# Kernel tuning notes

Hardware: AMD Instinct MI355X
Metric: run time of the kernel (lower is better)

## Reference

```python
import jax, jax.numpy as jnp
import numpy as np

B = 32768      # batch of pooled BEATs embeddings
D = 768        # d_model
H = 64         # bottleneck
E = 7          # number of machine types (experts)


def setup_inputs() -> dict:
    key = jax.random.key(0)
    k_x, k_id, k_w1, k_b1, k_w2, k_b2 = jax.random.split(key, 6)
    x = jax.random.normal(k_x, (B, D), dtype=jnp.float32)
    expert_ids = jax.random.randint(k_id, (B,), 0, E, dtype=jnp.int64)
    # per-expert bottleneck adapter params (Linear(D,H) -> ReLU -> Linear(H,D))
    s1 = 1.0 / np.sqrt(D)
    s2 = 1.0 / np.sqrt(H)
    W1 = jax.random.uniform(k_w1, (E, D, H), jnp.float32, -s1, s1)
    b1 = jax.random.uniform(k_b1, (E, H), jnp.float32, -s1, s1)
    W2 = jax.random.uniform(k_w2, (E, H, D), jnp.float32, -s2, s2)
    b2 = jax.random.uniform(k_b2, (E, D), jnp.float32, -s2, s2)
    return {"x": x, "expert_ids": expert_ids, "W1": W1, "b1": b1, "W2": W2, "b2": b2}


def reference(x, expert_ids, W1, b1, W2, b2):
    # out[i] = x[i] + adapter_{id[i]}(x[i]); hard one-hot routing.
    # E is small and fixed, so loop over experts and mask-select (vectorized over batch).
    out = x
    for e in range(E):
        h = jax.nn.relu(x @ W1[e] + b1[e])          # [B, H]
        y = h @ W2[e] + b2[e]                        # [B, D]
        mask = (expert_ids == e)[:, None]            # [B, 1]
        out = out + jnp.where(mask, y, jnp.zeros((), x.dtype))
    return out
```

## Files before the change

### kernel.cpp

```cpp
#include <hip/hip_runtime.h>

#define B_ROWS 32768
#define D_DIM 768
#define H_DIM 64
#define E_NUM 7
#define BM 64
#define PERM_CAP (B_ROWS + E_NUM * BM)
#define NBLOCKS_MAIN (PERM_CAP / BM)
#define W_ELEMS (E_NUM * D_DIM * H_DIM)

#define PREP_INIT ((PERM_CAP + 255) / 256)
#define PREP_W1 (E_NUM * 24)
#define PREP_W2 (E_NUM * 12)

#define WS_COUNTS 0
#define WS_BASE   64
#define WS_CURSOR 128
#define WS_PERM   256
#define WS_W      133120
#define WS_WF     1376256
#define WS_NEEDED (WS_W + 2 * WS_WF)

typedef __attribute__((ext_vector_type(8))) short short8;
typedef __attribute__((ext_vector_type(8))) __bf16 bf16x8;
typedef __attribute__((ext_vector_type(4))) float f32x4;

__device__ __forceinline__ unsigned short f2bf(float f) {
  unsigned int u = __float_as_uint(f);
  unsigned int r = (u + 0x7fffu + ((u >> 16) & 1u)) >> 16;
  return (unsigned short)r;
}
__device__ __forceinline__ float bf2f(unsigned short s) {
  return __uint_as_float(((unsigned int)s) << 16);
}
__device__ __forceinline__ f32x4 mfma16(short8 a, short8 b, f32x4 c) {
  return __builtin_amdgcn_mfma_f32_16x16x32_bf16(
      __builtin_bit_cast(bf16x8, a), __builtin_bit_cast(bf16x8, b), c, 0, 0, 0);
}

__global__ void k_prep(int* __restrict__ counts, int* __restrict__ perm,
                       const float* __restrict__ W1, const float* __restrict__ W2,
                       short* __restrict__ w1f, short* __restrict__ w2f) {
  __shared__ __align__(16) float tile[64][65];
  const int bid = blockIdx.x;
  const int t = threadIdx.x;

  if (bid < PREP_INIT) {
    int i = bid * 256 + t;
    if (i < PERM_CAP) perm[i] = -1;
    if (bid == 0 && t < 16) counts[t] = 0;
    return;
  }
  if (bid < PREP_INIT + PREP_W1) {
    const int b = bid - PREP_INIT;
    const int e = b / 24, kt = b % 24;
    {
      const int d = t >> 3, hc = (t & 7) * 8;
      const float* src = W1 + ((size_t)(e * D_DIM + kt * 32 + d)) * H_DIM + hc;
      f32x4 v0 = *reinterpret_cast<const f32x4*>(src);
      f32x4 v1 = *reinterpret_cast<const f32x4*>(src + 4);
#pragma unroll
      for (int i = 0; i < 4; ++i) {
        tile[d][hc + i] = v0[i];
        tile[d][hc + 4 + i] = v1[i];
      }
    }
    __syncthreads();
    {
      const int n = t >> 6, lane = t & 63;
      const int kgo = lane >> 4, l15o = lane & 15;
      short8 hi8, lo8;
#pragma unroll
      for (int j = 0; j < 8; ++j) {
        float v = tile[kgo * 8 + j][n * 16 + l15o];
        unsigned short h = f2bf(v);
        hi8[j] = (short)h;
        lo8[j] = (short)f2bf(v - bf2f(h));
      }
      short* dst = w1f + ((size_t)(((e * 4 + n) * 24 + kt) * 2) << 9) + (lane << 3);
      *reinterpret_cast<short8*>(dst) = hi8;
      *reinterpret_cast<short8*>(dst + 512) = lo8;
    }
    return;
  }
  {
    const int b = bid - PREP_INIT - PREP_W1;
    const int e = b / 12, ctb = b % 12;
    {
      const int h = t >> 2, dc = (t & 3) * 16;
      const float* src = W2 + ((size_t)(e * H_DIM + h)) * D_DIM + ctb * 64 + dc;
#pragma unroll
      for (int k = 0; k < 4; ++k) {
        f32x4 v = *reinterpret_cast<const f32x4*>(src + k * 4);
#pragma unroll
        for (int i = 0; i < 4; ++i) tile[h][dc + k * 4 + i] = v[i];
      }
    }
    __syncthreads();
    {
      const int ct4 = t >> 6, lane = t & 63;
      const int kgo = lane >> 4, l15o = lane & 15;
      const int ct = ctb * 4 + ct4;
#pragma unroll
      for (int ks = 0; ks < 2; ++ks) {
        short8 hi8, lo8;
#pragma unroll
        for (int j = 0; j < 8; ++j) {
          float v = tile[ks * 32 + kgo * 8 + j][ct4 * 16 + l15o];
          unsigned short h = f2bf(v);
          hi8[j] = (short)h;
          lo8[j] = (short)f2bf(v - bf2f(h));
        }
        short* dst = w2f + ((size_t)(((e * 48 + ct) * 2 + ks) * 2) << 9) + (lane << 3);
        *reinterpret_cast<short8*>(dst) = hi8;
        *reinterpret_cast<short8*>(dst + 512) = lo8;
      }
    }
    return;
  }
}

__global__ void k_hist(const int* __restrict__ eid, int* __restrict__ counts) {
  __shared__ int lc[E_NUM];
  if (threadIdx.x < E_NUM) lc[threadIdx.x] = 0;
  __syncthreads();
  int e = eid[blockIdx.x * 256 + threadIdx.x];
  e = e < 0 ? 0 : (e >= E_NUM ? E_NUM - 1 : e);
  atomicAdd(&lc[e], 1);
  __syncthreads();
  if (threadIdx.x < E_NUM) atomicAdd(&counts[threadIdx.x], lc[threadIdx.x]);
}

__global__ void k_scan(const int* __restrict__ counts, int* __restrict__ base,
                       int* __restrict__ cursor) {
  if (threadIdx.x == 0) {
    int run = 0;
    for (int e = 0; e < E_NUM; ++e) {
      base[e] = run;
      cursor[e] = run;
      run += ((counts[e] + BM - 1) / BM) * BM;
    }
    base[E_NUM] = run;
  }
}

__global__ void k_scatter(const int* __restrict__ eid, int* __restrict__ cursor,
                          int* __restrict__ perm) {
  __shared__ int lc[E_NUM];
  __shared__ int lb[E_NUM];
  if (threadIdx.x < E_NUM) lc[threadIdx.x] = 0;
  __syncthreads();
  int i = blockIdx.x * 256 + threadIdx.x;
  int e = eid[i];
  e = e < 0 ? 0 : (e >= E_NUM ? E_NUM - 1 : e);
  int lpos = atomicAdd(&lc[e], 1);
  __syncthreads();
  if (threadIdx.x < E_NUM) lb[threadIdx.x] = atomicAdd(&cursor[threadIdx.x], lc[threadIdx.x]);
  __syncthreads();
  perm[lb[e] + lpos] = i;
}

__global__ __launch_bounds__(512, 4) void k_adapter(
    const float* __restrict__ x, const float* __restrict__ b1,
    const float* __restrict__ b2, const short* __restrict__ w1f,
    const short* __restrict__ w2f, const int* __restrict__ base,
    const int* __restrict__ perm, float* __restrict__ out) {
  __shared__ __align__(16) short hl_hi[4][16][72];
  __shared__ __align__(16) short hl_lo[4][16][72];
  __shared__ __align__(16) float ldsT[8][16][68];

  const int tid = threadIdx.x;
  const int wid = tid >> 6;
  const int lane = tid & 63;
  const int l15 = lane & 15;
  const int kg = lane >> 4;
  const int r = wid & 3;
  const int half = wid >> 2;
  const int m0 = blockIdx.x * BM;

  int e = 0;
#pragma unroll
  for (int i = 1; i < E_NUM; ++i)
    if (m0 >= base[i]) e = i;

  const int ar = perm[m0 + r * 16 + l15];
  const float* xrow = x + (size_t)(ar < 0 ? 0 : ar) * D_DIM;
  const short* w1e = w1f + (size_t)e * 98304;
  const int n0 = half * 2, n1 = half * 2 + 1;
#define W1P(n_, kt_) (w1e + (((size_t)((n_)*24 + (kt_)) * 2) << 9) + (lane << 3))

  f32x4 acc1[2] = {{0.f, 0.f, 0.f, 0.f}, {0.f, 0.f, 0.f, 0.f}};

  f32x4 nxa = *reinterpret_cast<const f32x4*>(xrow + kg * 8);
  f32x4 nxb = *reinterpret_cast<const f32x4*>(xrow + kg * 8 + 4);
  short8 nb0 = *reinterpret_cast<const short8*>(W1P(n0, 0));
  short8 nb1 = *reinterpret_cast<const short8*>(W1P(n0, 0) + 512);
  short8 nb2 = *reinterpret_cast<const short8*>(W1P(n1, 0));
  short8 nb3 = *reinterpret_cast<const short8*>(W1P(n1, 0) + 512);

#pragma unroll
  for (int kt = 0; kt < 24; ++kt) {
    f32x4 xa = nxa, xb = nxb;
    short8 b0h = nb0, b0l = nb1, b1h = nb2, b1l = nb3;
    if (kt < 23) {
      const int k0 = (kt + 1) * 32 + kg * 8;
      nxa = *reinterpret_cast<const f32x4*>(xrow + k0);
      nxb = *reinterpret_cast<const f32x4*>(xrow + k0 + 4);
      nb0 = *reinterpret_cast<const short8*>(W1P(n0, kt + 1));
      nb1 = *reinterpret_cast<const short8*>(W1P(n0, kt + 1) + 512);
      nb2 = *reinterpret_cast<const short8*>(W1P(n1, kt + 1));
      nb3 = *reinterpret_cast<const short8*>(W1P(n1, kt + 1) + 512);
    }
    short8 ahi, alo;
#pragma unroll
    for (int i = 0; i < 4; ++i) {
      unsigned short h0 = f2bf(xa[i]);
      ahi[i] = (short)h0;
      alo[i] = (short)f2bf(xa[i] - bf2f(h0));
      unsigned short h1 = f2bf(xb[i]);
      ahi[4 + i] = (short)h1;
      alo[4 + i] = (short)f2bf(xb[i] - bf2f(h1));
    }
    acc1[0] = mfma16(ahi, b0h, acc1[0]);
    acc1[0] = mfma16(alo, b0h, acc1[0]);
    acc1[0] = mfma16(ahi, b0l, acc1[0]);
    acc1[1] = mfma16(ahi, b1h, acc1[1]);
    acc1[1] = mfma16(alo, b1h, acc1[1]);
    acc1[1] = mfma16(ahi, b1l, acc1[1]);
  }

#pragma unroll
  for (int nn = 0; nn < 2; ++nn) {
    const int col = (half * 2 + nn) * 16 + l15;
    const float bv = b1[e * H_DIM + col];
#pragma unroll
    for (int j = 0; j < 4; ++j) {
      float v = acc1[nn][j] + bv;
      v = v > 0.f ? v : 0.f;
      unsigned short hh = f2bf(v);
      hl_hi[r][kg * 4 + j][col] = (short)hh;
      hl_lo[r][kg * 4 + j][col] = (short)f2bf(v - bf2f(hh));
    }
  }

  const short* w2e = w2f + (size_t)e * 98304;
  const int ct0 = half * 24;
#define W2P(ct_, ks_) (w2e + (((size_t)((ct_)*2 + (ks_)) * 2) << 9) + (lane << 3))
  short8 nwh = *reinterpret_cast<const short8*>(W2P(ct0, 0));
  short8 nwl = *reinterpret_cast<const short8*>(W2P(ct0, 0) + 512);

  const int grow = perm[m0 + r * 16 + (lane >> 2)];

  __syncthreads();

  short8 a2h[2], a2l[2];
#pragma unroll
  for (int ks = 0; ks < 2; ++ks) {
    a2h[ks] = *reinterpret_cast<const short8*>(&hl_hi[r][l15][ks * 32 + kg * 8]);
    a2l[ks] = *reinterpret_cast<const short8*>(&hl_lo[r][l15][ks * 32 + kg * 8]);
  }

  const float* b2e = b2 + e * D_DIM;
  const int tr = lane >> 2, cq = lane & 3;
  const float* xr2 = x + (size_t)(grow < 0 ? 0 : grow) * D_DIM;
  float* orow = out + (size_t)(grow < 0 ? 0 : grow) * D_DIM;

#pragma unroll
  for (int g = 0; g < 6; ++g) {
    f32x4 acc2[4];
#pragma unroll
    for (int t = 0; t < 8; ++t) {
      const int ct4 = t >> 1, ks = t & 1;
      short8 wh = nwh, wl = nwl;
      if (!(g == 5 && t == 7)) {
        const int t2 = t + 1;
        const int g2 = (t2 == 8) ? g + 1 : g;
        const int tt = t2 & 7;
        const int nct = ct0 + g2 * 4 + (tt >> 1);
        const int nks = tt & 1;
        nwh = *reinterpret_cast<const short8*>(W2P(nct, nks));
        nwl = *reinterpret_cast<const short8*>(W2P(nct, nks) + 512);
      }
      if (ks == 0) acc2[ct4] = (f32x4){0.f, 0.f, 0.f, 0.f};
      acc2[ct4] = mfma16(a2h[ks], wh, acc2[ct4]);
      acc2[ct4] = mfma16(a2l[ks], wh, acc2[ct4]);
      acc2[ct4] = mfma16(a2h[ks], wl, acc2[ct4]);
    }
#pragma unroll
    for (int ct4 = 0; ct4 < 4; ++ct4)
#pragma unroll
      for (int j = 0; j < 4; ++j) ldsT[wid][kg * 4 + j][ct4 * 16 + l15] = acc2[ct4][j];
    asm volatile("s_waitcnt lgkmcnt(0)" ::: "memory");
    __builtin_amdgcn_sched_barrier(0);

    const int colbase = (half * 6 + g) * 64 + cq * 16;
    f32x4 y0 = *reinterpret_cast<const f32x4*>(&ldsT[wid][tr][cq * 16 + 0]);
    f32x4 y1 = *reinterpret_cast<const f32x4*>(&ldsT[wid][tr][cq * 16 + 4]);
    f32x4 y2 = *reinterpret_cast<const f32x4*>(&ldsT[wid][tr][cq * 16 + 8]);
    f32x4 y3 = *reinterpret_cast<const f32x4*>(&ldsT[wid][tr][cq * 16 + 12]);
    if (grow >= 0) {
#pragma unroll
      for (int k = 0; k < 4; ++k) {
        f32x4 y = k == 0 ? y0 : (k == 1 ? y1 : (k == 2 ? y2 : y3));
        f32x4 bv = *reinterpret_cast<const f32x4*>(b2e + colbase + k * 4);
        f32x4 xv = *reinterpret_cast<const f32x4*>(xr2 + colbase + k * 4);
        f32x4 o = y + bv + xv;
        *reinterpret_cast<f32x4*>(orow + colbase + k * 4) = o;
      }
    }
  }
#undef W1P
#undef W2P
}

__global__ void k_fallback(const float* __restrict__ x, const int* __restrict__ eid,
                           const float* __restrict__ W1, const float* __restrict__ b1,
                           const float* __restrict__ W2, const float* __restrict__ b2,
                           float* __restrict__ out) {
  __shared__ float xs[D_DIM];
  __shared__ float hs[H_DIM];
  const int row = blockIdx.x;
  int e = eid[row];
  e = e < 0 ? 0 : (e >= E_NUM ? E_NUM - 1 : e);
  const float* xr = x + (size_t)row * D_DIM;
  for (int i = threadIdx.x; i < D_DIM; i += 256) xs[i] = xr[i];
  __syncthreads();
  if (threadIdx.x < H_DIM) {
    const float* w = W1 + (size_t)e * D_DIM * H_DIM + threadIdx.x;
    float acc = b1[e * H_DIM + threadIdx.x];
    for (int d = 0; d < D_DIM; ++d) acc += xs[d] * w[(size_t)d * H_DIM];
    hs[threadIdx.x] = acc > 0.f ? acc : 0.f;
  }
  __syncthreads();
  for (int c = threadIdx.x; c < D_DIM; c += 256) {
    const float* w = W2 + (size_t)e * H_DIM * D_DIM + c;
    float acc = b2[e * D_DIM + c];
    for (int h = 0; h < H_DIM; ++h) acc += hs[h] * w[(size_t)h * D_DIM];
    out[(size_t)row * D_DIM + c] = xs[c] + acc;
  }
}

extern "C" void kernel_launch(void* const* d_in, const int* in_sizes, int n_in,
                              void* d_out, int out_size, void* d_ws, size_t ws_size,
                              hipStream_t stream) {
  const float* x = (const float*)d_in[0];
  const int* eid = (const int*)d_in[1];
  const float* W1 = (const float*)d_in[2];
  const float* b1 = (const float*)d_in[3];
  const float* W2 = (const float*)d_in[4];
  const float* b2 = (const float*)d_in[5];
  float* out = (float*)d_out;

  if (ws_size < (size_t)WS_NEEDED) {
    k_fallback<<<B_ROWS, 256, 0, stream>>>(x, eid, W1, b1, W2, b2, out);
    return;
  }

  char* ws = (char*)d_ws;
  int* counts = (int*)(ws + WS_COUNTS);
  int* base = (int*)(ws + WS_BASE);
  int* cursor = (int*)(ws + WS_CURSOR);
  int* perm = (int*)(ws + WS_PERM);
  short* w1f = (short*)(ws + WS_W);
  short* w2f = (short*)(ws + WS_W + WS_WF);

  k_prep<<<PREP_INIT + PREP_W1 + PREP_W2, 256, 0, stream>>>(counts, perm, W1, W2, w1f, w2f);
  k_hist<<<B_ROWS / 256, 256, 0, stream>>>(eid, counts);
  k_scan<<<1, 64, 0, stream>>>(counts, base, cursor);
  k_scatter<<<B_ROWS / 256, 256, 0, stream>>>(eid, cursor, perm);
  k_adapter<<<NBLOCKS_MAIN, 512, 0, stream>>>(x, b1, b2, w1f, w2f, base, perm, out);
}
```

Before: 294.0 us.

## Use single-wave 16-row tiles with async global-to-LDS staging of x rows

Replaces the 512-thread, 64-row-tile adapter kernel with one-wavefront blocks that each process 16 gathered rows across all 64 hidden units and all 768 output columns. The gathered x rows are now staged into double-buffered, XOR-swizzled LDS using global_load_lds with explicit vmcnt waits, and W1 fragments are double-buffered in registers. The residual x values for the second GEMM are prefetched one group ahead, and the inter-wave __syncthreads is removed. Each wave now streams the full W1/W2 expert weights for just 16 rows, which raises weight traffic per row, and per-expert tile padding now costs up to 15 rows instead of 63.

```diff
diff --git a/kernel.cpp b/kernel.cpp
--- a/kernel.cpp
+++ b/kernel.cpp
@@ -4,9 +4,9 @@
 #define D_DIM 768
 #define H_DIM 64
 #define E_NUM 7
-#define BM 64
+#define BM 16
 #define PERM_CAP (B_ROWS + E_NUM * BM)
-#define NBLOCKS_MAIN (PERM_CAP / BM)
+#define NTILES (PERM_CAP / BM)
 #define W_ELEMS (E_NUM * D_DIM * H_DIM)
 
 #define PREP_INIT ((PERM_CAP + 255) / 256)
@@ -17,7 +17,7 @@
 #define WS_BASE   64
 #define WS_CURSOR 128
 #define WS_PERM   256
-#define WS_W      133120
+#define WS_W      131840
 #define WS_WF     1376256
 #define WS_NEEDED (WS_W + 2 * WS_WF)
 
@@ -36,6 +36,11 @@
 __device__ __forceinline__ f32x4 mfma16(short8 a, short8 b, f32x4 c) {
   return __builtin_amdgcn_mfma_f32_16x16x32_bf16(
       __builtin_bit_cast(bf16x8, a), __builtin_bit_cast(bf16x8, b), c, 0, 0, 0);
+}
+__device__ __forceinline__ void gload_lds16(const float* g, void* l) {
+  __builtin_amdgcn_global_load_lds(
+      (const __attribute__((address_space(1))) unsigned int*)g,
+      (__attribute__((address_space(3))) unsigned int*)l, 16, 0, 0);
 }
 
 __global__ void k_prep(int* __restrict__ counts, int* __restrict__ perm,
@@ -160,22 +165,19 @@
   perm[lb[e] + lpos] = i;
 }
 
-__global__ __launch_bounds__(512, 4) void k_adapter(
+__global__ __launch_bounds__(64, 2) void k_adapter(
     const float* __restrict__ x, const float* __restrict__ b1,
     const float* __restrict__ b2, const short* __restrict__ w1f,
     const short* __restrict__ w2f, const int* __restrict__ base,
     const int* __restrict__ perm, float* __restrict__ out) {
-  __shared__ __align__(16) short hl_hi[4][16][72];
-  __shared__ __align__(16) short hl_lo[4][16][72];
-  __shared__ __align__(16) float ldsT[8][16][68];
-
-  const int tid = threadIdx.x;
-  const int wid = tid >> 6;
-  const int lane = tid & 63;
+  __shared__ __align__(16) float stg[2][2][16][32];
+  __shared__ __align__(16) short hl_hi[16][72];
+  __shared__ __align__(16) short hl_lo[16][72];
+  __shared__ __align__(16) float ldsT[16][68];
+
+  const int lane = threadIdx.x;
   const int l15 = lane & 15;
   const int kg = lane >> 4;
-  const int r = wid & 3;
-  const int half = wid >> 2;
   const int m0 = blockIdx.x * BM;
 
   int e = 0;
@@ -183,100 +185,134 @@
   for (int i = 1; i < E_NUM; ++i)
     if (m0 >= base[i]) e = i;
 
-  const int ar = perm[m0 + r * 16 + l15];
-  const float* xrow = x + (size_t)(ar < 0 ? 0 : ar) * D_DIM;
+  const int r8 = lane >> 3;
+  int pr0 = perm[m0 + r8];
+  int pr1 = perm[m0 + 8 + r8];
+  if (pr0 < 0) pr0 = 0;
+  if (pr1 < 0) pr1 = 0;
+  const int sc = ((lane & 7) ^ r8) * 4;
+  const float* sb0 = x + (size_t)pr0 * D_DIM + sc;
+  const float* sb1 = x + (size_t)pr1 * D_DIM + sc;
+
   const short* w1e = w1f + (size_t)e * 98304;
-  const int n0 = half * 2, n1 = half * 2 + 1;
-#define W1P(n_, kt_) (w1e + (((size_t)((n_)*24 + (kt_)) * 2) << 9) + (lane << 3))
-
-  f32x4 acc1[2] = {{0.f, 0.f, 0.f, 0.f}, {0.f, 0.f, 0.f, 0.f}};
-
-  f32x4 nxa = *reinterpret_cast<const f32x4*>(xrow + kg * 8);
-  f32x4 nxb = *reinterpret_cast<const f32x4*>(xrow + kg * 8 + 4);
-  short8 nb0 = *reinterpret_cast<const short8*>(W1P(n0, 0));
-  short8 nb1 = *reinterpret_cast<const short8*>(W1P(n0, 0) + 512);
-  short8 nb2 = *reinterpret_cast<const short8*>(W1P(n1, 0));
-  short8 nb3 = *reinterpret_cast<const short8*>(W1P(n1, 0) + 512);
-
-#pragma unroll
-  for (int kt = 0; kt < 24; ++kt) {
-    f32x4 xa = nxa, xb = nxb;
-    short8 b0h = nb0, b0l = nb1, b1h = nb2, b1l = nb3;
-    if (kt < 23) {
-      const int k0 = (kt + 1) * 32 + kg * 8;
-      nxa = *reinterpret_cast<const f32x4*>(xrow + k0);
-      nxb = *reinterpret_cast<const f32x4*>(xrow + k0 + 4);
-      nb0 = *reinterpret_cast<const short8*>(W1P(n0, kt + 1));
-      nb1 = *reinterpret_cast<const short8*>(W1P(n0, kt + 1) + 512);
-      nb2 = *reinterpret_cast<const short8*>(W1P(n1, kt + 1));
-      nb3 = *reinterpret_cast<const short8*>(W1P(n1, kt + 1) + 512);
-    }
-    short8 ahi, alo;
-#pragma unroll
-    for (int i = 0; i < 4; ++i) {
-      unsigned short h0 = f2bf(xa[i]);
-      ahi[i] = (short)h0;
-      alo[i] = (short)f2bf(xa[i] - bf2f(h0));
-      unsigned short h1 = f2bf(xb[i]);
-      ahi[4 + i] = (short)h1;
-      alo[4 + i] = (short)f2bf(xb[i] - bf2f(h1));
-    }
-    acc1[0] = mfma16(ahi, b0h, acc1[0]);
-    acc1[0] = mfma16(alo, b0h, acc1[0]);
-    acc1[0] = mfma16(ahi, b0l, acc1[0]);
-    acc1[1] = mfma16(ahi, b1h, acc1[1]);
-    acc1[1] = mfma16(alo, b1h, acc1[1]);
-    acc1[1] = mfma16(ahi, b1l, acc1[1]);
-  }
-
-#pragma unroll
-  for (int nn = 0; nn < 2; ++nn) {
-    const int col = (half * 2 + nn) * 16 + l15;
+
+#define STAGE_PAIR(p)                                                      \
+  {                                                                        \
+    char* db_ = (char*)&stg[(p) & 1][0][0][0];                             \
+    const int k0_ = (p) * 64;                                              \
+    gload_lds16(sb0 + k0_, db_ + lane * 16);                               \
+    gload_lds16(sb1 + k0_, db_ + 1024 + lane * 16);                        \
+    gload_lds16(sb0 + k0_ + 32, db_ + 2048 + lane * 16);                   \
+    gload_lds16(sb1 + k0_ + 32, db_ + 3072 + lane * 16);                   \
+  }
+
+#define LOAD_W1(kt, dst)                                                   \
+  {                                                                        \
+    _Pragma("unroll") for (int n_ = 0; n_ < 4; ++n_) {                     \
+      const short* p_ =                                                    \
+          w1e + (((size_t)(n_ * 24 + (kt)) * 2) << 9) + (lane << 3);       \
+      dst[n_][0] = *reinterpret_cast<const short8*>(p_);                   \
+      dst[n_][1] = *reinterpret_cast<const short8*>(p_ + 512);             \
+    }                                                                      \
+  }
+
+#define DO_KT(kt, w_)                                                      \
+  {                                                                        \
+    const int c0_ = (kg * 2) ^ (l15 & 7);                                  \
+    const float* sp_ = &stg[((kt) >> 1) & 1][(kt)&1][l15][0];              \
+    f32x4 va_ = *reinterpret_cast<const f32x4*>(sp_ + c0_ * 4);            \
+    f32x4 vb_ = *reinterpret_cast<const f32x4*>(sp_ + (c0_ ^ 1) * 4);      \
+    short8 ahi_, alo_;                                                     \
+    _Pragma("unroll") for (int i_ = 0; i_ < 4; ++i_) {                     \
+      unsigned short h0_ = f2bf(va_[i_]);                                  \
+      ahi_[i_] = (short)h0_;                                               \
+      alo_[i_] = (short)f2bf(va_[i_] - bf2f(h0_));                         \
+      unsigned short h1_ = f2bf(vb_[i_]);                                  \
+      ahi_[4 + i_] = (short)h1_;                                           \
+      alo_[4 + i_] = (short)f2bf(vb_[i_] - bf2f(h1_));                     \
+    }                                                                      \
+    _Pragma("unroll") for (int n_ = 0; n_ < 4; ++n_) {                     \
+      acc1[n_] = mfma16(ahi_, w_[n_][0], acc1[n_]);                        \
+      acc1[n_] = mfma16(alo_, w_[n_][0], acc1[n_]);                        \
+      acc1[n_] = mfma16(ahi_, w_[n_][1], acc1[n_]);                        \
+    }                                                                      \
+  }
+
+  f32x4 acc1[4] = {{0.f, 0.f, 0.f, 0.f},
+                   {0.f, 0.f, 0.f, 0.f},
+                   {0.f, 0.f, 0.f, 0.f},
+                   {0.f, 0.f, 0.f, 0.f}};
+  short8 wA[4][2], wB[4][2];
+
+  STAGE_PAIR(0);
+  __builtin_amdgcn_sched_barrier(0);
+  LOAD_W1(0, wA);
+  __builtin_amdgcn_sched_barrier(0);
+  STAGE_PAIR(1);
+  __builtin_amdgcn_sched_barrier(0);
+
+#pragma unroll
+  for (int p = 0; p < 12; ++p) {
+    asm volatile("s_waitcnt vmcnt(12)" ::: "memory");
+    __builtin_amdgcn_sched_barrier(0);
+    LOAD_W1(2 * p + 1, wB);
+    DO_KT(2 * p, wA);
+    if (2 * p + 2 < 24) LOAD_W1(2 * p + 2, wA);
+    DO_KT(2 * p + 1, wB);
+    __builtin_amdgcn_sched_barrier(0);
+    if (p + 2 < 12) STAGE_PAIR(p + 2);
+    __builtin_amdgcn_sched_barrier(0);
+  }
+
+#pragma unroll
+  for (int nn = 0; nn < 4; ++nn) {
+    const int col = nn * 16 + l15;
     const float bv = b1[e * H_DIM + col];
 #pragma unroll
     for (int j = 0; j < 4; ++j) {
       float v = acc1[nn][j] + bv;
       v = v > 0.f ? v : 0.f;
       unsigned short hh = f2bf(v);
-      hl_hi[r][kg * 4 + j][col] = (short)hh;
-      hl_lo[r][kg * 4 + j][col] = (short)f2bf(v - bf2f(hh));
-    }
+      hl_hi[kg * 4 + j][col] = (short)hh;
+      hl_lo[kg * 4 + j][col] = (short)f2bf(v - bf2f(hh));
+    }
+  }
+
+  short8 a2h[2], a2l[2];
+#pragma unroll
+  for (int ks = 0; ks < 2; ++ks) {
+    a2h[ks] = *reinterpret_cast<const short8*>(&hl_hi[l15][ks * 32 + kg * 8]);
+    a2l[ks] = *reinterpret_cast<const short8*>(&hl_lo[l15][ks * 32 + kg * 8]);
   }
 
   const short* w2e = w2f + (size_t)e * 98304;
-  const int ct0 = half * 24;
 #define W2P(ct_, ks_) (w2e + (((size_t)((ct_)*2 + (ks_)) * 2) << 9) + (lane << 3))
-  short8 nwh = *reinterpret_cast<const short8*>(W2P(ct0, 0));
-  short8 nwl = *reinterpret_cast<const short8*>(W2P(ct0, 0) + 512);
-
-  const int grow = perm[m0 + r * 16 + (lane >> 2)];
-
-  __syncthreads();
-
-  short8 a2h[2], a2l[2];
-#pragma unroll
-  for (int ks = 0; ks < 2; ++ks) {
-    a2h[ks] = *reinterpret_cast<const short8*>(&hl_hi[r][l15][ks * 32 + kg * 8]);
-    a2l[ks] = *reinterpret_cast<const short8*>(&hl_lo[r][l15][ks * 32 + kg * 8]);
-  }
-
-  const float* b2e = b2 + e * D_DIM;
+
   const int tr = lane >> 2, cq = lane & 3;
+  const int grow = perm[m0 + tr];
   const float* xr2 = x + (size_t)(grow < 0 ? 0 : grow) * D_DIM;
   float* orow = out + (size_t)(grow < 0 ? 0 : grow) * D_DIM;
-
-#pragma unroll
-  for (int g = 0; g < 6; ++g) {
+  const float* b2e = b2 + e * D_DIM;
+
+  short8 nwh = *reinterpret_cast<const short8*>(W2P(0, 0));
+  short8 nwl = *reinterpret_cast<const short8*>(W2P(0, 0) + 512);
+  f32x4 xva[4];
+#pragma unroll
+  for (int k = 0; k < 4; ++k)
+    xva[k] = *reinterpret_cast<const f32x4*>(xr2 + cq * 16 + k * 4);
+
+#pragma unroll
+  for (int g = 0; g < 12; ++g) {
     f32x4 acc2[4];
 #pragma unroll
     for (int t = 0; t < 8; ++t) {
       const int ct4 = t >> 1, ks = t & 1;
       short8 wh = nwh, wl = nwl;
-      if (!(g == 5 && t == 7)) {
+      if (!(g == 11 && t == 7)) {
         const int t2 = t + 1;
         const int g2 = (t2 == 8) ? g + 1 : g;
         const int tt = t2 & 7;
-        const int nct = ct0 + g2 * 4 + (tt >> 1);
+        const int nct = g2 * 4 + (tt >> 1);
         const int nks = tt & 1;
         nwh = *reinterpret_cast<const short8*>(W2P(nct, nks));
         nwl = *reinterpret_cast<const short8*>(W2P(nct, nks) + 512);
@@ -286,31 +322,35 @@
       acc2[ct4] = mfma16(a2l[ks], wh, acc2[ct4]);
       acc2[ct4] = mfma16(a2h[ks], wl, acc2[ct4]);
     }
+    f32x4 xcur[4];
+#pragma unroll
+    for (int k = 0; k < 4; ++k) xcur[k] = xva[k];
+    if (g < 11) {
+#pragma unroll
+      for (int k = 0; k < 4; ++k)
+        xva[k] = *reinterpret_cast<const f32x4*>(xr2 + (g + 1) * 64 + cq * 16 + k * 4);
+    }
 #pragma unroll
     for (int ct4 = 0; ct4 < 4; ++ct4)
 #pragma unroll
-      for (int j = 0; j < 4; ++j) ldsT[wid][kg * 4 + j][ct4 * 16 + l15] = acc2[ct4][j];
-    asm volatile("s_waitcnt lgkmcnt(0)" ::: "memory");
-    __builtin_amdgcn_sched_barrier(0);
-
-    const int colbase = (half * 6 + g) * 64 + cq * 16;
-    f32x4 y0 = *reinterpret_cast<const f32x4*>(&ldsT[wid][tr][cq * 16 + 0]);
-    f32x4 y1 = *reinterpret_cast<const f32x4*>(&ldsT[wid][tr][cq * 16 + 4]);
-    f32x4 y2 = *reinterpret_cast<const f32x4*>(&ldsT[wid][tr][cq * 16 + 8]);
-    f32x4 y3 = *reinterpret_cast<const f32x4*>(&ldsT[wid][tr][cq * 16 + 12]);
+      for (int j = 0; j < 4; ++j) ldsT[kg * 4 + j][ct4 * 16 + l15] = acc2[ct4][j];
+
+    const int colbase = g * 64 + cq * 16;
     if (grow >= 0) {
 #pragma unroll
       for (int k = 0; k < 4; ++k) {
-        f32x4 y = k == 0 ? y0 : (k == 1 ? y1 : (k == 2 ? y2 : y3));
+        f32x4 y = *reinterpret_cast<const f32x4*>(&ldsT[tr][cq * 16 + k * 4]);
         f32x4 bv = *reinterpret_cast<const f32x4*>(b2e + colbase + k * 4);
-        f32x4 xv = *reinterpret_cast<const f32x4*>(xr2 + colbase + k * 4);
-        f32x4 o = y + bv + xv;
+        f32x4 o = y + bv + xcur[k];
         *reinterpret_cast<f32x4*>(orow + colbase + k * 4) = o;
       }
     }
   }
 #undef W1P
 #undef W2P
+#undef STAGE_PAIR
+#undef LOAD_W1
+#undef DO_KT
 }
 
 __global__ void k_fallback(const float* __restrict__ x, const int* __restrict__ eid,
@@ -368,5 +408,5 @@
   k_hist<<<B_ROWS / 256, 256, 0, stream>>>(eid, counts);
   k_scan<<<1, 64, 0, stream>>>(counts, base, cursor);
   k_scatter<<<B_ROWS / 256, 256, 0, stream>>>(eid, cursor, perm);
-  k_adapter<<<NBLOCKS_MAIN, 512, 0, stream>>>(x, b1, b2, w1f, w2f, base, perm, out);
-}
+  k_adapter<<<NTILES, 64, 0, stream>>>(x, b1, b2, w1f, w2f, base, perm, out);
+}
```

After: 248.7 us. -15.4%, faster.
